# Kernel optimization log

Hardware: AMD Instinct MI355X
Metric: run time of the kernel (lower is better)

Reference implementation:

```python
import jax, jax.numpy as jnp
import numpy as np

D_K = 64
D_MODEL = 1024
N_HEADS = 16


def setup_inputs() -> dict:
    key = jax.random.key(0)
    ks = jax.random.split(key, 9)
    B, S = 2, 2048
    scale = 1.0 / np.sqrt(D_MODEL)
    inp = {
        "x": jax.random.normal(ks[0], (B, S, D_MODEL), dtype=jnp.float32),
        "w_q": jax.random.normal(ks[1], (D_MODEL, N_HEADS * D_K), dtype=jnp.float32) * scale,
        "b_q": jnp.zeros((N_HEADS * D_K,), dtype=jnp.float32),
        "w_k": jax.random.normal(ks[2], (D_MODEL, N_HEADS * D_K), dtype=jnp.float32) * scale,
        "b_k": jnp.zeros((N_HEADS * D_K,), dtype=jnp.float32),
        "w_v": jax.random.normal(ks[3], (D_MODEL, N_HEADS * D_K), dtype=jnp.float32) * scale,
        "b_v": jnp.zeros((N_HEADS * D_K,), dtype=jnp.float32),
        "w_o": jax.random.normal(ks[4], (N_HEADS * D_K, D_MODEL), dtype=jnp.float32) * scale,
        "b_o": jnp.zeros((D_MODEL,), dtype=jnp.float32),
    }
    return inp


def reference(x, w_q, b_q, w_k, b_k, w_v, b_v, w_o, b_o):
    B, S, _ = x.shape
    H, Dk = N_HEADS, D_K

    def split_heads(m):  # [B,S,H*Dk] -> [B,H,S,Dk]
        return m.reshape(B, S, H, Dk).transpose(0, 2, 1, 3)

    Q = split_heads(x @ w_q + b_q)
    K = split_heads(x @ w_k + b_k)
    V = split_heads(x @ w_v + b_v)

    scores = jnp.einsum("bhsd,bhtd->bhst", Q, K) / jnp.sqrt(jnp.float32(Dk))
    probs = jax.nn.softmax(scores, axis=-1)
    attn = jnp.einsum("bhst,bhtd->bhsd", probs, V)  # [B,H,S,Dk]
    attn = attn.transpose(0, 2, 1, 3).reshape(B, S, H * Dk)
    return attn @ w_o + b_o
```

## Files before the change

kernel.cpp:

```cpp
#include <hip/hip_runtime.h>
#include <math.h>

#define D_MODELc 1024
#define N_HEADSc 16
#define D_Kc     64
#define B_SZc    2
#define S_LENc   2048
#define NTOKc    (B_SZc * S_LENc)

using half8  = __attribute__((ext_vector_type(8))) _Float16;
using half4  = __attribute__((ext_vector_type(4))) _Float16;
using fp16x2 = __attribute__((ext_vector_type(2))) __fp16;
using float4v = __attribute__((ext_vector_type(4))) float;

__global__ __launch_bounds__(256) void cvt_all(
    const float* __restrict__ x,
    const float* __restrict__ W0, const float* __restrict__ W1,
    const float* __restrict__ W2, const float* __restrict__ W3,
    _Float16* __restrict__ wout, _Float16* __restrict__ xout)
{
    __shared__ float T[32][33];
    const int z = blockIdx.z;
    const int t = threadIdx.x;

    if (z == 4) {
        const int bid = blockIdx.y * 32 + blockIdx.x;
        #pragma unroll
        for (int c = 0; c < 2; ++c) {
            const int i = bid * 512 + c * 256 + t;
            float4v a = ((const float4v*)x)[2 * i];
            float4v b = ((const float4v*)x)[2 * i + 1];
            half8 h;
            h[0] = (_Float16)a[0]; h[1] = (_Float16)a[1];
            h[2] = (_Float16)a[2]; h[3] = (_Float16)a[3];
            h[4] = (_Float16)b[0]; h[5] = (_Float16)b[1];
            h[6] = (_Float16)b[2]; h[7] = (_Float16)b[3];
            ((half8*)xout)[i] = h;
        }
        return;
    }

    const float* W = (z == 0) ? W0 : (z == 1) ? W1 : (z == 2) ? W2 : W3;
    _Float16* O = wout + (size_t)z * 1024 * 1024;

    const int k0 = blockIdx.x * 32;
    const int n0 = blockIdx.y * 32;
    {
        const int r = t >> 3, c4 = (t & 7) * 4;
        float4v v = *(const float4v*)(W + (size_t)(k0 + r) * 1024 + n0 + c4);
        T[r][c4 + 0] = v[0]; T[r][c4 + 1] = v[1];
        T[r][c4 + 2] = v[2]; T[r][c4 + 3] = v[3];
    }
    __syncthreads();
    {
        const int rn = t >> 3, ck4 = (t & 7) * 4;
        half4 h;
        h[0] = (_Float16)T[ck4 + 0][rn];
        h[1] = (_Float16)T[ck4 + 1][rn];
        h[2] = (_Float16)T[ck4 + 2][rn];
        h[3] = (_Float16)T[ck4 + 3][rn];
        *(half4*)(O + (size_t)(n0 + rn) * 1024 + k0 + ck4) = h;
    }
}

__global__ __launch_bounds__(256) void gemm_qkv(
    const _Float16* __restrict__ A, const _Float16* __restrict__ BtAll,
    const float* __restrict__ bias0, const float* __restrict__ bias1,
    const float* __restrict__ bias2, _Float16* __restrict__ Cout)
{
    __shared__ _Float16 Als[2][128 * 32];
    __shared__ _Float16 Bls[2][128 * 32];

    constexpr int K = 1024;
    const int tid = threadIdx.x;
    const int m0  = blockIdx.x * 128;
    const int n0  = blockIdx.y * 128;
    const int z   = blockIdx.z;

    const _Float16* Bt  = BtAll + (size_t)z * 1024 * 1024;
    const float* bias   = (z == 0) ? bias0 : (z == 1) ? bias1 : bias2;
    const float qscale  = (z == 0) ? 0.18033688011112042f : 1.0f;

    const int wave = tid >> 6, lane = tid & 63;
    const int wr = wave >> 1, wc = wave & 1;
    const int quad = lane >> 4, l16 = lane & 15;

    float4v acc[4][4];
    #pragma unroll
    for (int i = 0; i < 4; ++i)
        #pragma unroll
        for (int j = 0; j < 4; ++j)
            acc[i][j] = (float4v){0.f, 0.f, 0.f, 0.f};

    for (int k0 = 0; k0 < K; k0 += 64) {
        #pragma unroll
        for (int c = 0; c < 2; ++c) {
            const int i   = c * 256 + tid;
            const int row = i >> 2, kc = i & 3;
            #pragma unroll
            for (int h = 0; h < 2; ++h) {
                __builtin_amdgcn_global_load_lds(
                    (const __attribute__((address_space(1))) void*)
                        (A + (size_t)(m0 + row) * K + k0 + h * 32 + kc * 8),
                    (__attribute__((address_space(3))) void*)(Als[h] + i * 8),
                    16, 0, 0);
                __builtin_amdgcn_global_load_lds(
                    (const __attribute__((address_space(1))) void*)
                        (Bt + (size_t)(n0 + row) * K + k0 + h * 32 + kc * 8),
                    (__attribute__((address_space(3))) void*)(Bls[h] + i * 8),
                    16, 0, 0);
            }
        }
        __syncthreads();

        half8 af[4][2], bf[4][2];
        #pragma unroll
        for (int i = 0; i < 4; ++i) {
            const int r = (wr * 64 + i * 16 + l16) * 32 + quad * 8;
            af[i][0] = *(const half8*)(Als[0] + r);
            af[i][1] = *(const half8*)(Als[1] + r);
        }
        #pragma unroll
        for (int j = 0; j < 4; ++j) {
            const int r = (wc * 64 + j * 16 + l16) * 32 + quad * 8;
            bf[j][0] = *(const half8*)(Bls[0] + r);
            bf[j][1] = *(const half8*)(Bls[1] + r);
        }
        #pragma unroll
        for (int i = 0; i < 4; ++i)
            #pragma unroll
            for (int j = 0; j < 4; ++j) {
                acc[i][j] = __builtin_amdgcn_mfma_f32_16x16x32_f16(
                    af[i][0], bf[j][0], acc[i][j], 0, 0, 0);
                acc[i][j] = __builtin_amdgcn_mfma_f32_16x16x32_f16(
                    af[i][1], bf[j][1], acc[i][j], 0, 0, 0);
            }
        __syncthreads();
    }

    if (z != 2) {
        #pragma unroll
        for (int i = 0; i < 4; ++i) {
            const int rbase = m0 + wr * 64 + i * 16 + quad * 4;
            #pragma unroll
            for (int j = 0; j < 4; ++j) {
                const int col = n0 + wc * 64 + j * 16 + l16;
                const float bv = bias[col];
                #pragma unroll
                for (int r = 0; r < 4; ++r) {
                    const float v = (acc[i][j][r] + bv) * qscale;
                    const int n = rbase + r;
                    const int b = n >> 11, s = n & 2047;
                    const int h = col >> 6, d = col & 63;
                    _Float16* C = Cout + (size_t)z * NTOKc * D_MODELc;
                    C[(((size_t)(b * N_HEADSc + h)) * S_LENc + s) * D_Kc + d] =
                        (_Float16)v;
                }
            }
        }
    } else {
        #pragma unroll
        for (int i = 0; i < 4; ++i) {
            const int rbase = m0 + wr * 64 + i * 16 + quad * 4;
            const int b = rbase >> 11, s0 = rbase & 2047;
            #pragma unroll
            for (int j = 0; j < 4; ++j) {
                const int col = n0 + wc * 64 + j * 16 + l16;
                const float bv = bias[col];
                const int h = col >> 6, d = col & 63;
                half4 hv;
                #pragma unroll
                for (int r = 0; r < 4; ++r)
                    hv[r] = (_Float16)(acc[i][j][r] + bv);
                _Float16* C = Cout + (size_t)2 * NTOKc * D_MODELc;
                *(half4*)(C + (((size_t)(b * N_HEADSc + h)) * D_Kc + d) *
                          S_LENc + s0) = hv;
            }
        }
    }
}

__global__ __launch_bounds__(256) void gemm_out(
    const _Float16* __restrict__ A, const _Float16* __restrict__ Bt,
    const float* __restrict__ bias, float* __restrict__ C)
{
    __shared__ _Float16 Als[2][64 * 32];
    __shared__ _Float16 Bls[2][128 * 32];

    constexpr int K = 1024;
    const int tid = threadIdx.x;
    const int m0  = blockIdx.x * 64;
    const int n0  = blockIdx.y * 128;

    const int wave = tid >> 6, lane = tid & 63;
    const int wr = wave >> 1, wc = wave & 1;
    const int quad = lane >> 4, l16 = lane & 15;

    float4v acc[2][4];
    #pragma unroll
    for (int i = 0; i < 2; ++i)
        #pragma unroll
        for (int j = 0; j < 4; ++j)
            acc[i][j] = (float4v){0.f, 0.f, 0.f, 0.f};

    for (int k0 = 0; k0 < K; k0 += 64) {
        {
            const int row = tid >> 2, kc = tid & 3;
            #pragma unroll
            for (int h = 0; h < 2; ++h)
                __builtin_amdgcn_global_load_lds(
                    (const __attribute__((address_space(1))) void*)
                        (A + (size_t)(m0 + row) * K + k0 + h * 32 + kc * 8),
                    (__attribute__((address_space(3))) void*)(Als[h] + tid * 8),
                    16, 0, 0);
        }
        #pragma unroll
        for (int c = 0; c < 2; ++c) {
            const int i = c * 256 + tid;
            const int row = i >> 2, kc = i & 3;
            #pragma unroll
            for (int h = 0; h < 2; ++h)
                __builtin_amdgcn_global_load_lds(
                    (const __attribute__((address_space(1))) void*)
                        (Bt + (size_t)(n0 + row) * K + k0 + h * 32 + kc * 8),
                    (__attribute__((address_space(3))) void*)(Bls[h] + i * 8),
                    16, 0, 0);
        }
        __syncthreads();

        half8 af[2][2], bf[4][2];
        #pragma unroll
        for (int i = 0; i < 2; ++i) {
            const int r = (wr * 32 + i * 16 + l16) * 32 + quad * 8;
            af[i][0] = *(const half8*)(Als[0] + r);
            af[i][1] = *(const half8*)(Als[1] + r);
        }
        #pragma unroll
        for (int j = 0; j < 4; ++j) {
            const int r = (wc * 64 + j * 16 + l16) * 32 + quad * 8;
            bf[j][0] = *(const half8*)(Bls[0] + r);
            bf[j][1] = *(const half8*)(Bls[1] + r);
        }
        #pragma unroll
        for (int i = 0; i < 2; ++i)
            #pragma unroll
            for (int j = 0; j < 4; ++j) {
                acc[i][j] = __builtin_amdgcn_mfma_f32_16x16x32_f16(
                    af[i][0], bf[j][0], acc[i][j], 0, 0, 0);
                acc[i][j] = __builtin_amdgcn_mfma_f32_16x16x32_f16(
                    af[i][1], bf[j][1], acc[i][j], 0, 0, 0);
            }
        __syncthreads();
    }

    #pragma unroll
    for (int i = 0; i < 2; ++i) {
        const int rbase = m0 + wr * 32 + i * 16 + quad * 4;
        #pragma unroll
        for (int j = 0; j < 4; ++j) {
            const int col = n0 + wc * 64 + j * 16 + l16;
            const float bv = bias[col];
            #pragma unroll
            for (int r = 0; r < 4; ++r)
                C[(size_t)(rbase + r) * 1024 + col] = acc[i][j][r] + bv;
        }
    }
}

__global__ __launch_bounds__(256) void attn_mfma(
    const _Float16* __restrict__ Qb, const _Float16* __restrict__ Kb,
    const _Float16* __restrict__ Vtg, _Float16* __restrict__ Op,
    float* __restrict__ Lp)
{
    constexpr int PS = 72;
    __shared__ _Float16 Ks[64 * PS];
    __shared__ _Float16 Vt[64 * PS];
    __shared__ _Float16 Ps[128 * PS];

    const int tid  = threadIdx.x;
    const int wv   = tid >> 6;
    const int lane = tid & 63;
    const int quad = lane >> 4;
    const int l16  = lane & 15;

    const int q0 = blockIdx.x * 128;
    const int bh = blockIdx.y;
    const int sp = blockIdx.z;
    const int kb = sp * (S_LENc / 2);
    const int kend = kb + S_LENc / 2;

    const _Float16* Qsl = Qb  + (size_t)bh * S_LENc * D_Kc;
    const _Float16* Ksl = Kb  + (size_t)bh * S_LENc * D_Kc;
    const _Float16* Vsl = Vtg + (size_t)bh * S_LENc * D_Kc;

    half8 aq[2][2];
    #pragma unroll
    for (int qf = 0; qf < 2; ++qf) {
        const int row = q0 + wv * 32 + qf * 16 + l16;
        aq[qf][0] = *(const half8*)(Qsl + (size_t)row * 64 + quad * 8);
        aq[qf][1] = *(const half8*)(Qsl + (size_t)row * 64 + 32 + quad * 8);
    }

    float4v O[2][4];
    #pragma unroll
    for (int qf = 0; qf < 2; ++qf)
        #pragma unroll
        for (int nt = 0; nt < 4; ++nt)
            O[qf][nt] = (float4v){0.f, 0.f, 0.f, 0.f};
    float lr[2] = {0.f, 0.f};

    const int sr = tid >> 2;
    const int sg = (tid & 3) * 16;

    for (int t0 = kb; t0 < kend; t0 += 64) {
        half8 k0 = *(const half8*)(Ksl + (size_t)(t0 + sr) * 64 + sg);
        half8 k1 = *(const half8*)(Ksl + (size_t)(t0 + sr) * 64 + sg + 8);
        half8 v0 = *(const half8*)(Vsl + (size_t)sr * S_LENc + t0 + sg);
        half8 v1 = *(const half8*)(Vsl + (size_t)sr * S_LENc + t0 + sg + 8);
        __syncthreads();
        *(half8*)(Ks + sr * PS + sg)     = k0;
        *(half8*)(Ks + sr * PS + sg + 8) = k1;
        *(half8*)(Vt + sr * PS + sg)     = v0;
        *(half8*)(Vt + sr * PS + sg + 8) = v1;
        __syncthreads();

        half8 kf[4][2];
        #pragma unroll
        for (int nt = 0; nt < 4; ++nt) {
            kf[nt][0] = *(const half8*)(Ks + (nt * 16 + l16) * PS + quad * 8);
            kf[nt][1] = *(const half8*)(Ks + (nt * 16 + l16) * PS + 32 + quad * 8);
        }

        #pragma unroll
        for (int qf = 0; qf < 2; ++qf) {
            float4v st[4];
            #pragma unroll
            for (int nt = 0; nt < 4; ++nt) {
                st[nt] = __builtin_amdgcn_mfma_f32_16x16x32_f16(
                    kf[nt][0], aq[qf][0], (float4v){0.f, 0.f, 0.f, 0.f}, 0, 0, 0);
                st[nt] = __builtin_amdgcn_mfma_f32_16x16x32_f16(
                    kf[nt][1], aq[qf][1], st[nt], 0, 0, 0);
            }
            float ls = 0.f;
            #pragma unroll
            for (int nt = 0; nt < 4; ++nt) {
                const float p0 = __builtin_amdgcn_exp2f(fminf(st[nt][0], 15.5f));
                const float p1 = __builtin_amdgcn_exp2f(fminf(st[nt][1], 15.5f));
                const float p2 = __builtin_amdgcn_exp2f(fminf(st[nt][2], 15.5f));
                const float p3 = __builtin_amdgcn_exp2f(fminf(st[nt][3], 15.5f));
                ls += (p0 + p1) + (p2 + p3);
                union { fp16x2 h2[2]; half4 h4; } u;
                u.h2[0] = __builtin_amdgcn_cvt_pkrtz(p0, p1);
                u.h2[1] = __builtin_amdgcn_cvt_pkrtz(p2, p3);
                *(half4*)(Ps + (wv * 32 + qf * 16 + l16) * PS +
                          nt * 16 + quad * 4) = u.h4;
            }
            lr[qf] += ls;
        }

        half8 bvv[4][2];
        #pragma unroll
        for (int nt = 0; nt < 4; ++nt) {
            bvv[nt][0] = *(const half8*)(Vt + (nt * 16 + l16) * PS + quad * 8);
            bvv[nt][1] = *(const half8*)(Vt + (nt * 16 + l16) * PS + 32 + quad * 8);
        }
        #pragma unroll
        for (int qf = 0; qf < 2; ++qf) {
            half8 ap0 = *(const half8*)(Ps + (wv * 32 + qf * 16 + l16) * PS + quad * 8);
            half8 ap1 = *(const half8*)(Ps + (wv * 32 + qf * 16 + l16) * PS + 32 + quad * 8);
            #pragma unroll
            for (int nt = 0; nt < 4; ++nt) {
                O[qf][nt] = __builtin_amdgcn_mfma_f32_16x16x32_f16(
                    ap0, bvv[nt][0], O[qf][nt], 0, 0, 0);
                O[qf][nt] = __builtin_amdgcn_mfma_f32_16x16x32_f16(
                    ap1, bvv[nt][1], O[qf][nt], 0, 0, 0);
            }
        }
    }

    const size_t qgb = (size_t)bh * S_LENc;
    #pragma unroll
    for (int qf = 0; qf < 2; ++qf) {
        float t = lr[qf];
        t += __shfl_xor(t, 16, 64);
        t += __shfl_xor(t, 32, 64);
        if (quad == 0)
            Lp[(size_t)sp * 65536 + qgb + q0 + wv * 32 + qf * 16 + l16] = t;
        #pragma unroll
        for (int r = 0; r < 4; ++r) {
            const int q = q0 + wv * 32 + qf * 16 + quad * 4 + r;
            _Float16* dst = Op + ((size_t)sp * 65536 + qgb + q) * 64;
            #pragma unroll
            for (int nt = 0; nt < 4; ++nt)
                dst[nt * 16 + l16] = (_Float16)O[qf][nt][r];
        }
    }
}

__global__ __launch_bounds__(256) void attn_combine(
    const _Float16* __restrict__ Op, const float* __restrict__ Lp,
    _Float16* __restrict__ Ab)
{
    const int i  = blockIdx.x * 256 + threadIdx.x;
    const int e0 = i * 8;
    const int qg = e0 >> 6;
    const int d0 = e0 & 63;
    const int bh = qg >> 11, q = qg & 2047;
    const int b  = bh >> 4,  h = bh & 15;

    const float inv = 1.0f / (Lp[qg] + Lp[65536 + qg]);
    half8 o0 = *(const half8*)(Op + (size_t)qg * 64 + d0);
    half8 o1 = *(const half8*)(Op + ((size_t)65536 + qg) * 64 + d0);
    half8 hv;
    #pragma unroll
    for (int j = 0; j < 8; ++j)
        hv[j] = (_Float16)(((float)o0[j] + (float)o1[j]) * inv);
    *(half8*)(Ab + ((size_t)(b * S_LENc + q)) * 1024 + h * 64 + d0) = hv;
}

extern "C" void kernel_launch(void* const* d_in, const int* in_sizes, int n_in,
                              void* d_out, int out_size, void* d_ws, size_t ws_size,
                              hipStream_t stream)
{
    const float* x  = (const float*)d_in[0];
    const float* wq = (const float*)d_in[1];
    const float* bq = (const float*)d_in[2];
    const float* wk = (const float*)d_in[3];
    const float* bk = (const float*)d_in[4];
    const float* wv = (const float*)d_in[5];
    const float* bv = (const float*)d_in[6];
    const float* wo = (const float*)d_in[7];
    const float* bo = (const float*)d_in[8];
    float* out = (float*)d_out;

    const size_t M1 = 1024 * 1024;
    const size_t M4 = 4 * M1;
    _Float16* xh = (_Float16*)d_ws;
    _Float16* wh = xh + M4;
    _Float16* Qh = wh + M4;
    _Float16* Oph = Qh + 3 * M4;
    float*    Lp  = (float*)(Oph + 2 * M4);
    _Float16* Ah = xh;

    cvt_all<<<dim3(32, 32, 5), dim3(256), 0, stream>>>(
        x, wq, wk, wv, wo, wh, xh);
    gemm_qkv<<<dim3(NTOKc / 128, D_MODELc / 128, 3), dim3(256), 0, stream>>>(
        xh, wh, bq, bk, bv, Qh);
    attn_mfma<<<dim3(S_LENc / 128, B_SZc * N_HEADSc, 2), dim3(256), 0, stream>>>(
        Qh, Qh + M4, Qh + 2 * M4, Oph, Lp);
    attn_combine<<<dim3(NTOKc * D_MODELc / 8 / 256), dim3(256), 0, stream>>>(
        Oph, Lp, Ah);
    gemm_out<<<dim3(NTOKc / 64, D_MODELc / 128), dim3(256), 0, stream>>>(
        Ah, wh + 3 * M1, bo, out);
}
```

Baseline: 206.1 us.

## Split attention keys four ways with XCD-aware block index remapping

Raises the key-dimension split in the flash attention kernel from 2 to 4, giving 2048 blocks instead of 1024 so the GPU is better filled. It flattens the grid to 1D and remaps block ids so that the low 3 bits (likely the XCD assignment) group blocks sharing the same head and split, which should improve L2 reuse of K/V. The combine kernel now sums four partial outputs and four softmax denominators, which adds extra partial-output traffic and workspace. The max handling is unchanged, which implies the partials share a fixed reference rather than per-split maxima.

```diff
diff --git a/kernel.cpp b/kernel.cpp
--- a/kernel.cpp
+++ b/kernel.cpp
@@ -7,6 +7,7 @@
 #define B_SZc    2
 #define S_LENc   2048
 #define NTOKc    (B_SZc * S_LENc)
+#define SPLITc   4
 
 using half8  = __attribute__((ext_vector_type(8))) _Float16;
 using half4  = __attribute__((ext_vector_type(4))) _Float16;
@@ -283,11 +284,17 @@
     const int quad = lane >> 4;
     const int l16  = lane & 15;
 
-    const int q0 = blockIdx.x * 128;
-    const int bh = blockIdx.y;
-    const int sp = blockIdx.z;
-    const int kb = sp * (S_LENc / 2);
-    const int kend = kb + S_LENc / 2;
+    const int id  = blockIdx.x;
+    const int cls = id & 7;
+    const int idx = id >> 3;
+    const int qi  = idx & 15;
+    const int c0  = ((idx >> 4) << 3) | cls;
+    const int bh  = c0 >> 2;
+    const int sp  = c0 & 3;
+
+    const int q0 = qi * 128;
+    const int kb = sp * (S_LENc / SPLITc);
+    const int kend = kb + S_LENc / SPLITc;
 
     const _Float16* Qsl = Qb  + (size_t)bh * S_LENc * D_Kc;
     const _Float16* Ksl = Kb  + (size_t)bh * S_LENc * D_Kc;
@@ -408,13 +415,21 @@
     const int bh = qg >> 11, q = qg & 2047;
     const int b  = bh >> 4,  h = bh & 15;
 
-    const float inv = 1.0f / (Lp[qg] + Lp[65536 + qg]);
-    half8 o0 = *(const half8*)(Op + (size_t)qg * 64 + d0);
-    half8 o1 = *(const half8*)(Op + ((size_t)65536 + qg) * 64 + d0);
+    float lsum = 0.f;
+    #pragma unroll
+    for (int s = 0; s < SPLITc; ++s) lsum += Lp[(size_t)s * 65536 + qg];
+    const float inv = 1.0f / lsum;
+
+    float acc[8] = {};
+    #pragma unroll
+    for (int s = 0; s < SPLITc; ++s) {
+        half8 o = *(const half8*)(Op + ((size_t)s * 65536 + qg) * 64 + d0);
+        #pragma unroll
+        for (int j = 0; j < 8; ++j) acc[j] += (float)o[j];
+    }
     half8 hv;
     #pragma unroll
-    for (int j = 0; j < 8; ++j)
-        hv[j] = (_Float16)(((float)o0[j] + (float)o1[j]) * inv);
+    for (int j = 0; j < 8; ++j) hv[j] = (_Float16)(acc[j] * inv);
     *(half8*)(Ab + ((size_t)(b * S_LENc + q)) * 1024 + h * 64 + d0) = hv;
 }
 
@@ -439,14 +454,15 @@
     _Float16* wh = xh + M4;
     _Float16* Qh = wh + M4;
     _Float16* Oph = Qh + 3 * M4;
-    float*    Lp  = (float*)(Oph + 2 * M4);
+    float*    Lp  = (float*)(Oph + SPLITc * M4);
     _Float16* Ah = xh;
 
     cvt_all<<<dim3(32, 32, 5), dim3(256), 0, stream>>>(
         x, wq, wk, wv, wo, wh, xh);
     gemm_qkv<<<dim3(NTOKc / 128, D_MODELc / 128, 3), dim3(256), 0, stream>>>(
         xh, wh, bq, bk, bv, Qh);
-    attn_mfma<<<dim3(S_LENc / 128, B_SZc * N_HEADSc, 2), dim3(256), 0, stream>>>(
+    attn_mfma<<<dim3((S_LENc / 128) * B_SZc * N_HEADSc * SPLITc), dim3(256),
+                0, stream>>>(
         Qh, Qh + M4, Qh + 2 * M4, Oph, Lp);
     attn_combine<<<dim3(NTOKc * D_MODELc / 8 / 256), dim3(256), 0, stream>>>(
         Oph, Lp, Ah);
```

Measured after the change: 213.3 us. 1.04x slower.
